# Kernel optimization log

Hardware: AMD Instinct MI355X
Metric: run time of the kernel (lower is better)

The kernel has to match this reference:

```python
import jax, jax.numpy as jnp
import numpy as np

TOP_K = 8
SCORE_FUNC = "sigmoid"
ROUTE_NORM = True
ROUTE_SCALE = 2.5


def setup_inputs() -> dict:
    key = jax.random.key(0)
    k1, k2, k3 = jax.random.split(key, 3)
    B, S, H, E = 4, 4096, 2048, 64
    hidden_states = jax.random.normal(k1, (B, S, H), dtype=jnp.float32)
    # nn.Linear default init scale ~ 1/sqrt(H); exact distribution irrelevant for correctness
    gate_w = jax.random.normal(k2, (E, H), dtype=jnp.float32) * (1.0 / np.sqrt(H))
    expert_bias = jax.random.normal(k3, (E,), dtype=jnp.float32) * 0.1
    return {"hidden_states": hidden_states, "expert_bias": expert_bias, "gate_w": gate_w}


def reference(hidden_states, expert_bias, gate_w):
    B, S, H = hidden_states.shape
    x = hidden_states.reshape(-1, H)  # [T, H]
    logits = jnp.einsum("th,eh->te", x, gate_w)  # [T, E]
    if SCORE_FUNC == "sigmoid":
        scores = jax.nn.sigmoid(logits.astype(jnp.float32))
    else:
        scores = jax.nn.softmax(logits.astype(jnp.float32), axis=-1)
    if expert_bias is not None:
        _, selected_experts = jax.lax.top_k(scores + expert_bias[None, :], TOP_K)
        top_scores = jnp.take_along_axis(scores, selected_experts, axis=1)
    else:
        top_scores, selected_experts = jax.lax.top_k(scores, TOP_K)
    if SCORE_FUNC == "sigmoid" and ROUTE_NORM:
        denom = jnp.sum(top_scores, axis=-1, keepdims=True) + 1e-20
        top_scores = top_scores / denom
    top_scores = top_scores * ROUTE_SCALE
    return top_scores, selected_experts
```

## Files before the change

kernel.cpp:

```cpp
#include <hip/hip_runtime.h>
#include <math.h>

#define T_TOTAL 16384
#define HDIM    2048
#define NEXP    64

template<int KS>
__global__ __launch_bounds__(256, 4)
void router_gemm_kernel(const float* __restrict__ x,
                        const float* __restrict__ w,
                        float* __restrict__ partial)
{
    constexpr int KSLICE = HDIM / KS;
    constexpr int BK    = 16;
    constexpr int XS_ST = 258;
    constexpr int WS_ST = 66;

    __shared__ float Xs[BK][XS_ST];
    __shared__ float Ws[BK][WS_ST];

    const int tid = threadIdx.x;
    const int tb  = blockIdx.x & 63;
    const int ks  = blockIdx.x >> 6;
    const int t0  = tb * 256;
    const int k0  = ks * KSLICE;

    const int kq  = tid & 3;
    const int rr  = tid >> 2;

    const int eg8 = (tid & 7) * 8;
    const int tg8 = (tid >> 3) * 8;

    float acc[8][8];
#pragma unroll
    for (int i = 0; i < 8; ++i)
#pragma unroll
        for (int j = 0; j < 8; ++j) acc[i][j] = 0.0f;

#pragma unroll 1
    for (int kc = 0; kc < KSLICE; kc += BK) {
        __syncthreads();

        {
            const float* xg = x + (size_t)t0 * HDIM + (k0 + kc) + kq * 4;
#pragma unroll
            for (int p = 0; p < 4; ++p) {
                const int r = p * 64 + rr;
                const float4 v = *(const float4*)(xg + (size_t)r * HDIM);
                Xs[kq * 4 + 0][r] = v.x;
                Xs[kq * 4 + 1][r] = v.y;
                Xs[kq * 4 + 2][r] = v.z;
                Xs[kq * 4 + 3][r] = v.w;
            }
        }
        {
            const float4 v = *(const float4*)(w + (size_t)rr * HDIM + (k0 + kc) + kq * 4);
            Ws[kq * 4 + 0][rr] = v.x;
            Ws[kq * 4 + 1][rr] = v.y;
            Ws[kq * 4 + 2][rr] = v.z;
            Ws[kq * 4 + 3][rr] = v.w;
        }
        __syncthreads();

#pragma unroll
        for (int k = 0; k < BK; ++k) {
            float xv[8], wv[8];
#pragma unroll
            for (int i = 0; i < 8; ++i) xv[i] = Xs[k][tg8 + i];
#pragma unroll
            for (int j = 0; j < 8; ++j) wv[j] = Ws[k][eg8 + j];
#pragma unroll
            for (int i = 0; i < 8; ++i)
#pragma unroll
                for (int j = 0; j < 8; ++j)
                    acc[i][j] = fmaf(xv[i], wv[j], acc[i][j]);
        }
    }

    float* pp = partial + ((size_t)(t0 + tg8) * KS + ks) * NEXP + eg8;
#pragma unroll
    for (int i = 0; i < 8; ++i) {
        float* q = pp + (size_t)i * KS * NEXP;
        *(float4*)(q)     = make_float4(acc[i][0], acc[i][1], acc[i][2], acc[i][3]);
        *(float4*)(q + 4) = make_float4(acc[i][4], acc[i][5], acc[i][6], acc[i][7]);
    }
}

__global__ __launch_bounds__(256)
void router_topk_kernel(const float* __restrict__ partial,
                        const float* __restrict__ bias,
                        float* __restrict__ out_scores,
                        float* __restrict__ out_idx,
                        int ksCount)
{
    const int token = blockIdx.x * 4 + (threadIdx.x >> 6);
    const int lane  = threadIdx.x & 63;

    const float* pt = partial + (size_t)token * ksCount * NEXP + lane;
    float logit = 0.0f;
    for (int s = 0; s < ksCount; ++s) logit += pt[(size_t)s * NEXP];

    const float score = 1.0f / (1.0f + expf(-logit));
    float key = score + bias[lane];

    float myscore = 0.0f;
    int   myidx   = 0;
    float denom   = 0.0f;

#pragma unroll
    for (int r = 0; r < 8; ++r) {
        float bk = key;
        int   bi = lane;
#pragma unroll
        for (int off = 32; off > 0; off >>= 1) {
            const float ok = __shfl_xor(bk, off);
            const int   oi = __shfl_xor(bi, off);
            if (ok > bk || (ok == bk && oi < bi)) { bk = ok; bi = oi; }
        }
        const float wsc = __shfl(score, bi);
        denom += wsc;
        if (lane == r)  { myscore = wsc; myidx = bi; }
        if (lane == bi) key = -__builtin_inff();
    }

    const float factor = 2.5f / (denom + 1e-20f);
    if (lane < 8) {
        out_scores[(size_t)token * 8 + lane] = myscore * factor;
        out_idx  [(size_t)token * 8 + lane] = (float)myidx;
    }
}

extern "C" void kernel_launch(void* const* d_in, const int* in_sizes, int n_in,
                              void* d_out, int out_size, void* d_ws, size_t ws_size,
                              hipStream_t stream)
{
    const float* x    = (const float*)d_in[0];
    const float* bias = (const float*)d_in[1];
    const float* w    = (const float*)d_in[2];

    float* out     = (float*)d_out;
    float* partial = (float*)d_ws;

    const size_t bytesPerSlice = (size_t)T_TOTAL * NEXP * 4;

    int ksCount;
    if (ws_size >= 16 * bytesPerSlice) {
        ksCount = 16;
        router_gemm_kernel<16><<<dim3(64 * 16), dim3(256), 0, stream>>>(x, w, partial);
    } else {
        ksCount = 4;
        router_gemm_kernel<4><<<dim3(64 * 4), dim3(256), 0, stream>>>(x, w, partial);
    }

    router_topk_kernel<<<dim3(T_TOTAL / 4), dim3(256), 0, stream>>>(
        partial, bias, out, out + (size_t)T_TOTAL * 8, ksCount);
}
```

Before: 253.5 us.

## Register-prefetch next K tile in router GEMM, widen BK, reduce split-K to 8

```diff
diff --git a/kernel.cpp b/kernel.cpp
--- a/kernel.cpp
+++ b/kernel.cpp
@@ -6,15 +6,15 @@
 #define NEXP    64
 
 template<int KS>
-__global__ __launch_bounds__(256, 4)
+__global__ __launch_bounds__(256, 2)
 void router_gemm_kernel(const float* __restrict__ x,
                         const float* __restrict__ w,
                         float* __restrict__ partial)
 {
     constexpr int KSLICE = HDIM / KS;
-    constexpr int BK    = 16;
-    constexpr int XS_ST = 258;
-    constexpr int WS_ST = 66;
+    constexpr int BK     = 32;
+    constexpr int XS_ST  = 258;
+    constexpr int WS_ST  = 66;
 
     __shared__ float Xs[BK][XS_ST];
     __shared__ float Ws[BK][WS_ST];
@@ -37,32 +37,61 @@
 #pragma unroll
         for (int j = 0; j < 8; ++j) acc[i][j] = 0.0f;
 
+    const float* xg = x + (size_t)t0 * HDIM + k0 + kq * 8;
+    const float* wg = w + (size_t)rr * HDIM + k0 + kq * 8;
+
+    float4 px[4][2];
+    float4 pw[2];
+
+#pragma unroll
+    for (int p = 0; p < 4; ++p) {
+        const float* src = xg + (size_t)(p * 64 + rr) * HDIM;
+        px[p][0] = *(const float4*)(src);
+        px[p][1] = *(const float4*)(src + 4);
+    }
+    pw[0] = *(const float4*)(wg);
+    pw[1] = *(const float4*)(wg + 4);
+
 #pragma unroll 1
     for (int kc = 0; kc < KSLICE; kc += BK) {
         __syncthreads();
 
-        {
-            const float* xg = x + (size_t)t0 * HDIM + (k0 + kc) + kq * 4;
+#pragma unroll
+        for (int p = 0; p < 4; ++p) {
+            const int r = p * 64 + rr;
+            Xs[kq * 8 + 0][r] = px[p][0].x;
+            Xs[kq * 8 + 1][r] = px[p][0].y;
+            Xs[kq * 8 + 2][r] = px[p][0].z;
+            Xs[kq * 8 + 3][r] = px[p][0].w;
+            Xs[kq * 8 + 4][r] = px[p][1].x;
+            Xs[kq * 8 + 5][r] = px[p][1].y;
+            Xs[kq * 8 + 6][r] = px[p][1].z;
+            Xs[kq * 8 + 7][r] = px[p][1].w;
+        }
+        Ws[kq * 8 + 0][rr] = pw[0].x;
+        Ws[kq * 8 + 1][rr] = pw[0].y;
+        Ws[kq * 8 + 2][rr] = pw[0].z;
+        Ws[kq * 8 + 3][rr] = pw[0].w;
+        Ws[kq * 8 + 4][rr] = pw[1].x;
+        Ws[kq * 8 + 5][rr] = pw[1].y;
+        Ws[kq * 8 + 6][rr] = pw[1].z;
+        Ws[kq * 8 + 7][rr] = pw[1].w;
+
+        __syncthreads();
+
+        if (kc + BK < KSLICE) {
+            const float* xn = xg + (kc + BK);
 #pragma unroll
             for (int p = 0; p < 4; ++p) {
-                const int r = p * 64 + rr;
-                const float4 v = *(const float4*)(xg + (size_t)r * HDIM);
-                Xs[kq * 4 + 0][r] = v.x;
-                Xs[kq * 4 + 1][r] = v.y;
-                Xs[kq * 4 + 2][r] = v.z;
-                Xs[kq * 4 + 3][r] = v.w;
+                const float* src = xn + (size_t)(p * 64 + rr) * HDIM;
+                px[p][0] = *(const float4*)(src);
+                px[p][1] = *(const float4*)(src + 4);
             }
+            pw[0] = *(const float4*)(wg + kc + BK);
+            pw[1] = *(const float4*)(wg + kc + BK + 4);
         }
-        {
-            const float4 v = *(const float4*)(w + (size_t)rr * HDIM + (k0 + kc) + kq * 4);
-            Ws[kq * 4 + 0][rr] = v.x;
-            Ws[kq * 4 + 1][rr] = v.y;
-            Ws[kq * 4 + 2][rr] = v.z;
-            Ws[kq * 4 + 3][rr] = v.w;
-        }
-        __syncthreads();
 
-#pragma unroll
+#pragma unroll 8
         for (int k = 0; k < BK; ++k) {
             float xv[8], wv[8];
 #pragma unroll
@@ -86,19 +115,20 @@
     }
 }
 
+template<int KS>
 __global__ __launch_bounds__(256)
 void router_topk_kernel(const float* __restrict__ partial,
                         const float* __restrict__ bias,
                         float* __restrict__ out_scores,
-                        float* __restrict__ out_idx,
-                        int ksCount)
+                        float* __restrict__ out_idx)
 {
     const int token = blockIdx.x * 4 + (threadIdx.x >> 6);
     const int lane  = threadIdx.x & 63;
 
-    const float* pt = partial + (size_t)token * ksCount * NEXP + lane;
+    const float* pt = partial + (size_t)token * KS * NEXP + lane;
     float logit = 0.0f;
-    for (int s = 0; s < ksCount; ++s) logit += pt[(size_t)s * NEXP];
+#pragma unroll
+    for (int s = 0; s < KS; ++s) logit += pt[(size_t)s * NEXP];
 
     const float score = 1.0f / (1.0f + expf(-logit));
     float key = score + bias[lane];
@@ -143,15 +173,13 @@
 
     const size_t bytesPerSlice = (size_t)T_TOTAL * NEXP * 4;
 
-    int ksCount;
-    if (ws_size >= 16 * bytesPerSlice) {
-        ksCount = 16;
-        router_gemm_kernel<16><<<dim3(64 * 16), dim3(256), 0, stream>>>(x, w, partial);
+    if (ws_size >= 8 * bytesPerSlice) {
+        router_gemm_kernel<8><<<dim3(64 * 8), dim3(256), 0, stream>>>(x, w, partial);
+        router_topk_kernel<8><<<dim3(T_TOTAL / 4), dim3(256), 0, stream>>>(
+            partial, bias, out, out + (size_t)T_TOTAL * 8);
     } else {
-        ksCount = 4;
         router_gemm_kernel<4><<<dim3(64 * 4), dim3(256), 0, stream>>>(x, w, partial);
+        router_topk_kernel<4><<<dim3(T_TOTAL / 4), dim3(256), 0, stream>>>(
+            partial, bias, out, out + (size_t)T_TOTAL * 8);
     }
-
-    router_topk_kernel<<<dim3(T_TOTAL / 4), dim3(256), 0, stream>>>(
-        partial, bias, out, out + (size_t)T_TOTAL * 8, ksCount);
 }
```

New measurement: 233.0 us. 8.1% less time.

## Replace FP32 FMA router GEMM with split-bf16 MFMA emulation

Applied to the files above, without the earlier changes.

```diff
diff --git a/kernel.cpp b/kernel.cpp
--- a/kernel.cpp
+++ b/kernel.cpp
@@ -4,101 +4,169 @@
 #define T_TOTAL 16384
 #define HDIM    2048
 #define NEXP    64
+#define KS_MAIN 4
+
+typedef unsigned short ushort_t;
+using bf16x8 = __attribute__((ext_vector_type(8))) short;
+using f32x4  = __attribute__((ext_vector_type(4))) float;
+
+__device__ __forceinline__ unsigned bf16rne(float f) {
+    const unsigned u = __float_as_uint(f);
+    return (u + 0x7FFFu + ((u >> 16) & 1u)) >> 16;
+}
+__device__ __forceinline__ float bf16tof(unsigned b) {
+    return __uint_as_float(b << 16);
+}
+
+__device__ __forceinline__ void split8(const float4 a, const float4 b,
+                                       bf16x8& h, bf16x8& m, bf16x8& l) {
+    float f[8] = {a.x, a.y, a.z, a.w, b.x, b.y, b.z, b.w};
+    unsigned hb[8], mb[8], lb[8];
+#pragma unroll
+    for (int j = 0; j < 8; ++j) {
+        const float    x  = f[j];
+        const unsigned hu = bf16rne(x);
+        const float    r1 = x - bf16tof(hu);
+        const unsigned mu = bf16rne(r1);
+        const float    r2 = r1 - bf16tof(mu);
+        const unsigned lu = bf16rne(r2);
+        hb[j] = hu; mb[j] = mu; lb[j] = lu;
+    }
+    union { unsigned u[4]; bf16x8 v; } H, M, L;
+#pragma unroll
+    for (int d = 0; d < 4; ++d) {
+        H.u[d] = hb[2*d] | (hb[2*d+1] << 16);
+        M.u[d] = mb[2*d] | (mb[2*d+1] << 16);
+        L.u[d] = lb[2*d] | (lb[2*d+1] << 16);
+    }
+    h = H.v; m = M.v; l = L.v;
+}
+
+__global__ void convert_w_kernel(const float* __restrict__ w,
+                                 ushort_t* __restrict__ whi,
+                                 ushort_t* __restrict__ wmid,
+                                 ushort_t* __restrict__ wlo)
+{
+    const int i = (blockIdx.x * 256 + threadIdx.x) * 4;
+    const float4 v = *(const float4*)(w + i);
+    float f[4] = {v.x, v.y, v.z, v.w};
+#pragma unroll
+    for (int j = 0; j < 4; ++j) {
+        const float    x  = f[j];
+        const unsigned hu = bf16rne(x);
+        const float    r1 = x - bf16tof(hu);
+        const unsigned mu = bf16rne(r1);
+        const float    r2 = r1 - bf16tof(mu);
+        const unsigned lu = bf16rne(r2);
+        whi [i + j] = (ushort_t)hu;
+        wmid[i + j] = (ushort_t)mu;
+        wlo [i + j] = (ushort_t)lu;
+    }
+}
+
+__global__ __launch_bounds__(256)
+void router_gemm_mfma(const float*   __restrict__ x,
+                      const ushort_t* __restrict__ whi,
+                      const ushort_t* __restrict__ wmid,
+                      const ushort_t* __restrict__ wlo,
+                      float* __restrict__ partial)
+{
+    const int tid  = threadIdx.x;
+    const int wv   = tid >> 6;
+    const int lane = tid & 63;
+    const int tb   = blockIdx.x >> 2;
+    const int ks   = blockIdx.x & 3;
+    const int t0   = tb * 128 + wv * 32;
+    const int k0   = ks * (HDIM / KS_MAIN);
+    const int lr   = lane & 15;
+    const int lg   = lane >> 4;
+    const int kl   = lg * 8;
+
+    f32x4 acc[2][4];
+#pragma unroll
+    for (int mt = 0; mt < 2; ++mt)
+#pragma unroll
+        for (int nt = 0; nt < 4; ++nt) {
+            f32x4 z = {0.0f, 0.0f, 0.0f, 0.0f};
+            acc[mt][nt] = z;
+        }
+
+    const float* px0 = x + (size_t)(t0 + lr) * HDIM + k0 + kl;
+    const float* px1 = px0 + (size_t)16 * HDIM;
+
+    const size_t boff = (size_t)lr * HDIM + k0 + kl;
+    const ushort_t* pbh = whi  + boff;
+    const ushort_t* pbm = wmid + boff;
+    const ushort_t* pbl = wlo  + boff;
+
+    for (int kk = 0; kk < HDIM / KS_MAIN; kk += 32) {
+        const float4 x00 = *(const float4*)(px0 + kk);
+        const float4 x01 = *(const float4*)(px0 + kk + 4);
+        const float4 x10 = *(const float4*)(px1 + kk);
+        const float4 x11 = *(const float4*)(px1 + kk + 4);
+
+        bf16x8 Ah[2], Am[2], Al[2];
+        split8(x00, x01, Ah[0], Am[0], Al[0]);
+        split8(x10, x11, Ah[1], Am[1], Al[1]);
+
+#pragma unroll
+        for (int nt = 0; nt < 4; ++nt) {
+            const size_t no = (size_t)nt * 16 * HDIM + kk;
+            const bf16x8 Bh = *(const bf16x8*)(pbh + no);
+            const bf16x8 Bm = *(const bf16x8*)(pbm + no);
+            const bf16x8 Bl = *(const bf16x8*)(pbl + no);
+#pragma unroll
+            for (int mt = 0; mt < 2; ++mt) {
+                acc[mt][nt] = __builtin_amdgcn_mfma_f32_16x16x32_bf16(Ah[mt], Bh, acc[mt][nt], 0, 0, 0);
+                acc[mt][nt] = __builtin_amdgcn_mfma_f32_16x16x32_bf16(Am[mt], Bh, acc[mt][nt], 0, 0, 0);
+                acc[mt][nt] = __builtin_amdgcn_mfma_f32_16x16x32_bf16(Al[mt], Bh, acc[mt][nt], 0, 0, 0);
+                acc[mt][nt] = __builtin_amdgcn_mfma_f32_16x16x32_bf16(Ah[mt], Bm, acc[mt][nt], 0, 0, 0);
+                acc[mt][nt] = __builtin_amdgcn_mfma_f32_16x16x32_bf16(Am[mt], Bm, acc[mt][nt], 0, 0, 0);
+                acc[mt][nt] = __builtin_amdgcn_mfma_f32_16x16x32_bf16(Ah[mt], Bl, acc[mt][nt], 0, 0, 0);
+            }
+        }
+    }
+
+#pragma unroll
+    for (int mt = 0; mt < 2; ++mt) {
+        const int trow = t0 + mt * 16 + lg * 4;
+#pragma unroll
+        for (int nt = 0; nt < 4; ++nt) {
+            float* pb = partial + ((size_t)trow * KS_MAIN + ks) * NEXP + nt * 16 + lr;
+#pragma unroll
+            for (int r = 0; r < 4; ++r)
+                pb[(size_t)r * KS_MAIN * NEXP] = acc[mt][nt][r];
+        }
+    }
+}
+
+__global__ void router_gemm_naive(const float* __restrict__ x,
+                                  const float* __restrict__ w,
+                                  float* __restrict__ partial)
+{
+    const int t = blockIdx.x;
+    const int e = threadIdx.x;
+    const float* xp = x + (size_t)t * HDIM;
+    const float* wp = w + (size_t)e * HDIM;
+    float s = 0.0f;
+    for (int k = 0; k < HDIM; ++k) s = fmaf(xp[k], wp[k], s);
+    partial[(size_t)t * NEXP + e] = s;
+}
 
 template<int KS>
-__global__ __launch_bounds__(256, 4)
-void router_gemm_kernel(const float* __restrict__ x,
-                        const float* __restrict__ w,
-                        float* __restrict__ partial)
-{
-    constexpr int KSLICE = HDIM / KS;
-    constexpr int BK    = 16;
-    constexpr int XS_ST = 258;
-    constexpr int WS_ST = 66;
-
-    __shared__ float Xs[BK][XS_ST];
-    __shared__ float Ws[BK][WS_ST];
-
-    const int tid = threadIdx.x;
-    const int tb  = blockIdx.x & 63;
-    const int ks  = blockIdx.x >> 6;
-    const int t0  = tb * 256;
-    const int k0  = ks * KSLICE;
-
-    const int kq  = tid & 3;
-    const int rr  = tid >> 2;
-
-    const int eg8 = (tid & 7) * 8;
-    const int tg8 = (tid >> 3) * 8;
-
-    float acc[8][8];
-#pragma unroll
-    for (int i = 0; i < 8; ++i)
-#pragma unroll
-        for (int j = 0; j < 8; ++j) acc[i][j] = 0.0f;
-
-#pragma unroll 1
-    for (int kc = 0; kc < KSLICE; kc += BK) {
-        __syncthreads();
-
-        {
-            const float* xg = x + (size_t)t0 * HDIM + (k0 + kc) + kq * 4;
-#pragma unroll
-            for (int p = 0; p < 4; ++p) {
-                const int r = p * 64 + rr;
-                const float4 v = *(const float4*)(xg + (size_t)r * HDIM);
-                Xs[kq * 4 + 0][r] = v.x;
-                Xs[kq * 4 + 1][r] = v.y;
-                Xs[kq * 4 + 2][r] = v.z;
-                Xs[kq * 4 + 3][r] = v.w;
-            }
-        }
-        {
-            const float4 v = *(const float4*)(w + (size_t)rr * HDIM + (k0 + kc) + kq * 4);
-            Ws[kq * 4 + 0][rr] = v.x;
-            Ws[kq * 4 + 1][rr] = v.y;
-            Ws[kq * 4 + 2][rr] = v.z;
-            Ws[kq * 4 + 3][rr] = v.w;
-        }
-        __syncthreads();
-
-#pragma unroll
-        for (int k = 0; k < BK; ++k) {
-            float xv[8], wv[8];
-#pragma unroll
-            for (int i = 0; i < 8; ++i) xv[i] = Xs[k][tg8 + i];
-#pragma unroll
-            for (int j = 0; j < 8; ++j) wv[j] = Ws[k][eg8 + j];
-#pragma unroll
-            for (int i = 0; i < 8; ++i)
-#pragma unroll
-                for (int j = 0; j < 8; ++j)
-                    acc[i][j] = fmaf(xv[i], wv[j], acc[i][j]);
-        }
-    }
-
-    float* pp = partial + ((size_t)(t0 + tg8) * KS + ks) * NEXP + eg8;
-#pragma unroll
-    for (int i = 0; i < 8; ++i) {
-        float* q = pp + (size_t)i * KS * NEXP;
-        *(float4*)(q)     = make_float4(acc[i][0], acc[i][1], acc[i][2], acc[i][3]);
-        *(float4*)(q + 4) = make_float4(acc[i][4], acc[i][5], acc[i][6], acc[i][7]);
-    }
-}
-
 __global__ __launch_bounds__(256)
 void router_topk_kernel(const float* __restrict__ partial,
                         const float* __restrict__ bias,
                         float* __restrict__ out_scores,
-                        float* __restrict__ out_idx,
-                        int ksCount)
+                        float* __restrict__ out_idx)
 {
     const int token = blockIdx.x * 4 + (threadIdx.x >> 6);
     const int lane  = threadIdx.x & 63;
 
-    const float* pt = partial + (size_t)token * ksCount * NEXP + lane;
+    const float* pt = partial + (size_t)token * KS * NEXP + lane;
     float logit = 0.0f;
-    for (int s = 0; s < ksCount; ++s) logit += pt[(size_t)s * NEXP];
+#pragma unroll
+    for (int s = 0; s < KS; ++s) logit += pt[(size_t)s * NEXP];
 
     const float score = 1.0f / (1.0f + expf(-logit));
     float key = score + bias[lane];
@@ -141,17 +209,23 @@
     float* out     = (float*)d_out;
     float* partial = (float*)d_ws;
 
-    const size_t bytesPerSlice = (size_t)T_TOTAL * NEXP * 4;
-
-    int ksCount;
-    if (ws_size >= 16 * bytesPerSlice) {
-        ksCount = 16;
-        router_gemm_kernel<16><<<dim3(64 * 16), dim3(256), 0, stream>>>(x, w, partial);
+    const size_t partialBytes = (size_t)T_TOTAL * KS_MAIN * NEXP * 4;
+    const size_t wplaneElems  = (size_t)NEXP * HDIM;
+    const size_t needBytes    = partialBytes + 3 * wplaneElems * sizeof(ushort_t);
+
+    if (ws_size >= needBytes) {
+        ushort_t* whi  = (ushort_t*)((char*)d_ws + partialBytes);
+        ushort_t* wmid = whi  + wplaneElems;
+        ushort_t* wlo  = wmid + wplaneElems;
+
+        convert_w_kernel<<<dim3(128), dim3(256), 0, stream>>>(w, whi, wmid, wlo);
+        router_gemm_mfma<<<dim3(128 * KS_MAIN), dim3(256), 0, stream>>>(
+            x, whi, wmid, wlo, partial);
+        router_topk_kernel<KS_MAIN><<<dim3(T_TOTAL / 4), dim3(256), 0, stream>>>(
+            partial, bias, out, out + (size_t)T_TOTAL * 8);
     } else {
-        ksCount = 4;
-        router_gemm_kernel<4><<<dim3(64 * 4), dim3(256), 0, stream>>>(x, w, partial);
-    }
-
-    router_topk_kernel<<<dim3(T_TOTAL / 4), dim3(256), 0, stream>>>(
-        partial, bias, out, out + (size_t)T_TOTAL * 8, ksCount);
-}
+        router_gemm_naive<<<dim3(T_TOTAL), dim3(64), 0, stream>>>(x, w, partial);
+        router_topk_kernel<1><<<dim3(T_TOTAL / 4), dim3(256), 0, stream>>>(
+            partial, bias, out, out + (size_t)T_TOTAL * 8);
+    }
+}
```

New measurement: 257.1 us. Within noise of the previous version (+1.4%).
